# Kernel optimization log

Hardware: AMD Instinct MI355X
Metric: run time of the kernel (lower is better)

The kernel has to match this reference:

```python
import jax, jax.numpy as jnp
import numpy as np

B, N, DIM = 4, 4096, 1024
HEADS, DIM_HEAD = 16, 64
DIM_INNER = HEADS * DIM_HEAD
ATTN_SCALE = 8.0
EPS = 1e-12  # F.normalize default eps


def setup_inputs() -> dict:
    key = jax.random.key(0)
    k1, k2, k3, k4, k5 = jax.random.split(key, 5)
    x = jax.random.normal(k1, (B, N, DIM), dtype=jnp.float32)
    gamma = jnp.ones((DIM,), dtype=jnp.float32)
    # stored as (in, out) so forward is x @ w
    w_qkv = jax.random.normal(k2, (DIM, 3 * DIM_INNER), dtype=jnp.float32) * (DIM ** -0.5)
    temperature = jnp.ones((HEADS, 1, 1), dtype=jnp.float32)
    w_out = jax.random.normal(k3, (DIM_INNER, DIM), dtype=jnp.float32) * (DIM_INNER ** -0.5)
    return {"x": x, "gamma": gamma, "w_qkv": w_qkv, "temperature": temperature, "w_out": w_out}


def _l2norm(t):
    # F.normalize(t, dim=-1): t / max(||t||_2, eps)
    n = jnp.linalg.norm(t, axis=-1, keepdims=True)
    return t / jnp.maximum(n, EPS)


def reference(x, gamma, w_qkv, temperature, w_out):
    b, n, dim = x.shape
    # RMSNorm: F.normalize(x, dim=-1) * sqrt(dim) * gamma
    xn = _l2norm(x) * (dim ** 0.5) * gamma
    # QKV projection -> qkv b h d n
    qkv = (xn @ w_qkv).reshape(b, n, 3, HEADS, DIM_HEAD)
    qkv = qkv.transpose(2, 0, 3, 4, 1)  # (3, b, h, d, n)
    q, k, v = qkv[0], qkv[1], qkv[2]
    # l2-normalize q, k over the sequence (last) axis; temperature-scale q
    q = _l2norm(q) * jnp.exp(temperature)  # temperature: (h,1,1) broadcast
    k = _l2norm(k)
    # cross-covariance attention over the small channel dim d
    sim = jnp.einsum('bhdn,bhen->bhde', q, k) * ATTN_SCALE
    attn = jax.nn.softmax(sim, axis=-1)
    out = jnp.einsum('bhde,bhen->bhdn', attn, v)
    # b h d n -> b n (h d), then out projection
    out = out.transpose(0, 3, 1, 2).reshape(b, n, DIM_INNER)
    return out @ w_out
```

## Files before the change

kernel.cpp:

```cpp
#include <hip/hip_runtime.h>
#include <stdint.h>

typedef unsigned short u16;
typedef unsigned int u32;
typedef __attribute__((ext_vector_type(8))) __bf16 bf16x8;
typedef __attribute__((ext_vector_type(4))) float f32x4;

#define M_TOT 16384
#define DIMX  1024

__device__ __forceinline__ u16 f2b(float f) {
  u32 u = __builtin_bit_cast(u32, f);
  u32 r = (u + 0x7fffu + ((u >> 16) & 1u)) >> 16;
  return (u16)r;
}

__device__ __forceinline__ void gl2lds16(const void* g, void* l) {
  __builtin_amdgcn_global_load_lds((const __attribute__((address_space(1))) void*)g,
                                   (__attribute__((address_space(3))) void*)l,
                                   16, 0, 0);
}

__global__ __launch_bounds__(256) void k_rms(const float* __restrict__ x,
                                             const float* __restrict__ gamma,
                                             u16* __restrict__ xn) {
  int row = blockIdx.x;
  int t = threadIdx.x;
  const float4* xr = (const float4*)(x + (size_t)row * DIMX);
  float4 v = xr[t];
  float ss = v.x * v.x + v.y * v.y + v.z * v.z + v.w * v.w;
#pragma unroll
  for (int o = 32; o > 0; o >>= 1) ss += __shfl_xor(ss, o, 64);
  __shared__ float wss[4];
  int w = t >> 6;
  if ((t & 63) == 0) wss[w] = ss;
  __syncthreads();
  float tot = wss[0] + wss[1] + wss[2] + wss[3];
  float scale = 32.0f / fmaxf(sqrtf(tot), 1e-12f);
  float4 g = ((const float4*)gamma)[t];
  ushort4 o4;
  o4.x = f2b(v.x * scale * g.x);
  o4.y = f2b(v.y * scale * g.y);
  o4.z = f2b(v.z * scale * g.z);
  o4.w = f2b(v.w * scale * g.w);
  ((ushort4*)xn)[(size_t)row * 256 + t] = o4;
}

__global__ __launch_bounds__(256) void k_castT(const float* __restrict__ in,
                                               u16* __restrict__ out, int Rr, int Cc) {
  __shared__ float tile[32][33];
  int c0 = blockIdx.x * 32, r0 = blockIdx.y * 32;
  int tx = threadIdx.x, ty = threadIdx.y;
#pragma unroll
  for (int i = 0; i < 4; i++)
    tile[ty + i * 8][tx] = in[(size_t)(r0 + ty + i * 8) * Cc + c0 + tx];
  __syncthreads();
#pragma unroll
  for (int i = 0; i < 4; i++)
    out[(size_t)(c0 + ty + i * 8) * Rr + r0 + tx] = f2b(tile[tx][ty + i * 8]);
}


template<bool SWAP>
__device__ __forceinline__ f32x4 mf(bf16x8 a, bf16x8 b, f32x4 c) {
  return SWAP ? __builtin_amdgcn_mfma_f32_16x16x32_bf16(b, a, c, 0, 0, 0)
              : __builtin_amdgcn_mfma_f32_16x16x32_bf16(a, b, c, 0, 0, 0);
}

__device__ __forceinline__ void stage_half(const u16* __restrict__ g,
                                           u16* dst, int t, int k0) {
#pragma unroll
  for (int r = 0; r < 2; r++) {
    int chunk = r * 512 + t;
    int row = chunk >> 3;
    int cc = (chunk & 7) ^ (row & 7);
    gl2lds16(g + (size_t)row * 1024 + (k0 + cc * 8),
             dst + (r * 512 + (t >> 6) * 64) * 8);
  }
}

template<bool SWAP>
__device__ __forceinline__ void gemm_core256(const u16* __restrict__ Ag,
                                             const u16* __restrict__ Bg,
                                             u16* lds, int t, f32x4 (&acc)[8][4]) {
  const int lane = t & 63;
  const int r16 = lane & 15, q = lane >> 4;
  const int s0 = (q ^ (r16 & 7)) * 8;
  const int wr = (t >> 6) >> 2, wc = (t >> 6) & 3;
  const int arow = wr * 16 + r16;
  const int brow = wc * 16 + r16;

  stage_half(Ag,              lds + 0,     t, 0);
  stage_half(Bg,              lds + 16384, t, 0);
  stage_half(Bg + 128 * 1024, lds + 24576, t, 0);
  stage_half(Ag + 128 * 1024, lds + 8192,  t, 0);
  asm volatile("s_waitcnt vmcnt(4)" ::: "memory");
  __builtin_amdgcn_s_barrier();

  bf16x8 af[4][2], bl[2][2], bh[2][2];
#pragma unroll 1
  for (int tt = 0; tt < 16; tt++) {
    const int bo = (tt & 1) << 15;
    const int nb = bo ^ 32768;
    const int k1 = ((tt + 1) & 15) << 6;
    const u16* A0 = lds + bo;
    const u16* A1 = lds + bo + 8192;
    const u16* B0 = lds + bo + 16384;
    const u16* B1 = lds + bo + 24576;

#pragma unroll
    for (int i = 0; i < 4; i++) {
      af[i][0] = *(const bf16x8*)(A0 + (i * 32 + arow) * 64 + s0);
      af[i][1] = *(const bf16x8*)(A0 + (i * 32 + arow) * 64 + (s0 ^ 32));
    }
#pragma unroll
    for (int j = 0; j < 2; j++) {
      bl[j][0] = *(const bf16x8*)(B0 + (j * 64 + brow) * 64 + s0);
      bl[j][1] = *(const bf16x8*)(B0 + (j * 64 + brow) * 64 + (s0 ^ 32));
    }
    stage_half(Ag, lds + nb, t, k1);
    __builtin_amdgcn_s_setprio(1);
#pragma unroll
    for (int kq = 0; kq < 2; kq++)
#pragma unroll
      for (int i = 0; i < 4; i++)
#pragma unroll
        for (int j = 0; j < 2; j++)
          acc[i][j] = mf<SWAP>(af[i][kq], bl[j][kq], acc[i][j]);
    __builtin_amdgcn_s_setprio(0);
    asm volatile("s_waitcnt vmcnt(4)" ::: "memory");
    __builtin_amdgcn_s_barrier();

#pragma unroll
    for (int j = 0; j < 2; j++) {
      bh[j][0] = *(const bf16x8*)(B1 + (j * 64 + brow) * 64 + s0);
      bh[j][1] = *(const bf16x8*)(B1 + (j * 64 + brow) * 64 + (s0 ^ 32));
    }
    stage_half(Bg, lds + nb + 16384, t, k1);
    __builtin_amdgcn_s_setprio(1);
#pragma unroll
    for (int kq = 0; kq < 2; kq++)
#pragma unroll
      for (int i = 0; i < 4; i++)
#pragma unroll
        for (int j = 0; j < 2; j++)
          acc[i][2 + j] = mf<SWAP>(af[i][kq], bh[j][kq], acc[i][2 + j]);
    __builtin_amdgcn_s_setprio(0);
    asm volatile("s_waitcnt vmcnt(4)" ::: "memory");
    __builtin_amdgcn_s_barrier();

#pragma unroll
    for (int i = 0; i < 4; i++) {
      af[i][0] = *(const bf16x8*)(A1 + (i * 32 + arow) * 64 + s0);
      af[i][1] = *(const bf16x8*)(A1 + (i * 32 + arow) * 64 + (s0 ^ 32));
    }
    stage_half(Bg + 128 * 1024, lds + nb + 24576, t, k1);
    __builtin_amdgcn_s_setprio(1);
#pragma unroll
    for (int kq = 0; kq < 2; kq++)
#pragma unroll
      for (int i = 0; i < 4; i++)
#pragma unroll
        for (int j = 0; j < 2; j++)
          acc[4 + i][j] = mf<SWAP>(af[i][kq], bl[j][kq], acc[4 + i][j]);
    __builtin_amdgcn_s_setprio(0);
    __builtin_amdgcn_s_barrier();

    stage_half(Ag + 128 * 1024, lds + nb + 8192, t, k1);
    __builtin_amdgcn_s_setprio(1);
#pragma unroll
    for (int kq = 0; kq < 2; kq++)
#pragma unroll
      for (int i = 0; i < 4; i++)
#pragma unroll
        for (int j = 0; j < 2; j++)
          acc[4 + i][2 + j] = mf<SWAP>(af[i][kq], bh[j][kq], acc[4 + i][2 + j]);
    __builtin_amdgcn_s_setprio(0);
    asm volatile("s_waitcnt vmcnt(4)" ::: "memory");
    __builtin_amdgcn_s_barrier();
  }
}

__global__ __launch_bounds__(512, 2) void k_gemm1(const u16* __restrict__ A,
                                                  const u16* __restrict__ Bt,
                                                  u16* __restrict__ qkT,
                                                  u16* __restrict__ vmat,
                                                  float* __restrict__ sumsq) {
  __shared__ u16 lds[8 * 8192];
  int l = blockIdx.x;
  int xcd = l & 7, c = l >> 3;
  int mt = xcd * 8 + (c & 7);
  int nt = c >> 3;
  int m0 = mt * 256, n0 = nt * 256;
  int t = threadIdx.x, lane = t & 63;
  int r16 = lane & 15, q = lane >> 4;
  int wr = (t >> 6) >> 2, wc = (t >> 6) & 3;
  f32x4 acc[8][4] = {};
  if (n0 < 2048) {
    gemm_core256<false>(A + (size_t)m0 * 1024, Bt + (size_t)n0 * 1024, lds, t, acc);
    int b = m0 >> 12;
#pragma unroll
    for (int j = 0; j < 4; j++) {
      int cc = n0 + j * 64 + wc * 16 + r16;
      float colss = 0.f;
#pragma unroll
      for (int i = 0; i < 8; i++) {
        f32x4 a = acc[i][j];
        colss += a.x * a.x + a.y * a.y + a.z * a.z + a.w * a.w;
        int m = m0 + i * 32 + wr * 16 + q * 4;
        ushort4 o4;
        o4.x = f2b(a.x); o4.y = f2b(a.y); o4.z = f2b(a.z); o4.w = f2b(a.w);
        *(ushort4*)(qkT + (size_t)cc * M_TOT + m) = o4;
      }
      colss += __shfl_xor(colss, 16, 64);
      colss += __shfl_xor(colss, 32, 64);
      if (lane < 16) atomicAdd(&sumsq[b * 2048 + cc], colss);
    }
  } else {
    gemm_core256<true>(A + (size_t)m0 * 1024, Bt + (size_t)n0 * 1024, lds, t, acc);
    int vc0 = n0 - 2048;
#pragma unroll
    for (int i = 0; i < 8; i++) {
      int m = m0 + i * 32 + wr * 16 + r16;
#pragma unroll
      for (int j = 0; j < 4; j++) {
        int cc = vc0 + j * 64 + wc * 16 + q * 4;
        f32x4 a = acc[i][j];
        ushort4 o4;
        o4.x = f2b(a.x); o4.y = f2b(a.y); o4.z = f2b(a.z); o4.w = f2b(a.w);
        *(ushort4*)(vmat + (size_t)m * 1024 + cc) = o4;
      }
    }
  }
}

__global__ __launch_bounds__(256) void k_attn_s(const u16* __restrict__ qkT,
                                                float* __restrict__ Spart) {
  __shared__ u16 Ql[64 * 256];
  __shared__ u16 Kl[64 * 256];
  int bh = blockIdx.x, split = blockIdx.y;
  int b = bh >> 4, h = bh & 15;
  int t = threadIdx.x, lane = t & 63, w = t >> 6;
  int r16 = lane & 15, q = lane >> 4;
  const u16* qbase = qkT + (size_t)(h * 64) * M_TOT + b * 4096 + split * 1024;
  const u16* kbase = qkT + (size_t)(1024 + h * 64) * M_TOT + b * 4096 + split * 1024;
  int drow = w * 16 + r16;
  f32x4 acc[4] = {};
#pragma unroll 1
  for (int it = 0; it < 4; it++) {
    int ncol = it * 256;
#pragma unroll
    for (int r = 0; r < 8; r++) {
      int ch = r * 256 + t;
      int row = ch >> 5;
      int sl = (ch & 31) ^ (row & 31);
      gl2lds16(qbase + (size_t)row * M_TOT + ncol + sl * 8,
               Ql + (r * 256 + w * 64) * 8);
      gl2lds16(kbase + (size_t)row * M_TOT + ncol + sl * 8,
               Kl + (r * 256 + w * 64) * 8);
    }
    asm volatile("s_waitcnt vmcnt(0)" ::: "memory");
    __syncthreads();
#pragma unroll
    for (int it2 = 0; it2 < 8; it2++) {
      bf16x8 aq = *(const bf16x8*)(Ql + drow * 256 + (((it2 * 4 + q) ^ (drow & 31)) * 8));
#pragma unroll
      for (int j = 0; j < 4; j++) {
        int erow = j * 16 + r16;
        bf16x8 bk = *(const bf16x8*)(Kl + erow * 256 + (((it2 * 4 + q) ^ (erow & 31)) * 8));
        acc[j] = __builtin_amdgcn_mfma_f32_16x16x32_bf16(bk, aq, acc[j], 0, 0, 0);
      }
    }
    __syncthreads();
  }
  float* Sp = Spart + ((size_t)split * 64 + bh) * 4096;
#pragma unroll
  for (int j = 0; j < 4; j++)
    *(f32x4*)(Sp + drow * 64 + j * 16 + q * 4) = acc[j];
}

__global__ __launch_bounds__(256) void k_softmax(const float* __restrict__ Spart,
                                                 const float* __restrict__ sumsq,
                                                 const float* __restrict__ temp,
                                                 u16* __restrict__ PT) {
  int bh = blockIdx.x;
  int b = bh >> 4, h = bh & 15;
  int t = threadIdx.x;
  int d = t & 63, w = t >> 6;
  int e0 = w * 16;
  __shared__ float rnk[64];
  __shared__ float redm[4][64];
  __shared__ float reds[4][64];
  if (t < 64) rnk[t] = 1.0f / fmaxf(sqrtf(sumsq[b * 2048 + 1024 + h * 64 + t]), 1e-12f);
  __syncthreads();
  float nq = sqrtf(sumsq[b * 2048 + h * 64 + d]);
  float qs = 8.0f * __expf(temp[h]) / fmaxf(nq, 1e-12f);
  const float* Sp = Spart + (size_t)bh * 4096 + d * 64 + e0;
  float vals[16];
#pragma unroll
  for (int e = 0; e < 16; e += 4) {
    f32x4 v = {};
#pragma unroll
    for (int s = 0; s < 4; s++)
      v += *(const f32x4*)(Sp + (size_t)s * 64 * 4096 + e);
    vals[e + 0] = v.x; vals[e + 1] = v.y; vals[e + 2] = v.z; vals[e + 3] = v.w;
  }
  float mx = -3.0e38f;
#pragma unroll
  for (int e = 0; e < 16; e++) {
    float v = vals[e] * qs * rnk[e0 + e];
    vals[e] = v;
    mx = fmaxf(mx, v);
  }
  redm[w][d] = mx;
  __syncthreads();
  float M = fmaxf(fmaxf(redm[0][d], redm[1][d]), fmaxf(redm[2][d], redm[3][d]));
  float s = 0.f;
#pragma unroll
  for (int e = 0; e < 16; e++) {
    float v = __expf(vals[e] - M);
    vals[e] = v;
    s += v;
  }
  reds[w][d] = s;
  __syncthreads();
  float inv = 1.0f / (reds[0][d] + reds[1][d] + reds[2][d] + reds[3][d]);
#pragma unroll
  for (int e = 0; e < 16; e++)
    PT[((size_t)bh * 64 + e0 + e) * 64 + d] = f2b(vals[e] * inv);
}

__global__ __launch_bounds__(256) void k_m(const u16* __restrict__ woT,
                                           const u16* __restrict__ PT,
                                           u16* __restrict__ MT) {
  int bh = blockIdx.x;
  int b = bh >> 4, h = bh & 15;
  int o0 = blockIdx.y * 128;
  int t = threadIdx.x, lane = t & 63, w = t >> 6;
  int r16 = lane & 15, q = lane >> 4;
  const u16* pbase = PT + (size_t)bh * 4096;
  f32x4 acc[2][4] = {};
#pragma unroll
  for (int ks = 0; ks < 2; ks++) {
    int kk = ks * 32 + q * 8;
    bf16x8 af[2], bfr[4];
#pragma unroll
    for (int i = 0; i < 2; i++)
      af[i] = *(const bf16x8*)(woT + (size_t)(o0 + w * 32 + i * 16 + r16) * 1024 + h * 64 + kk);
#pragma unroll
    for (int j = 0; j < 4; j++)
      bfr[j] = *(const bf16x8*)(pbase + (size_t)(j * 16 + r16) * 64 + kk);
#pragma unroll
    for (int i = 0; i < 2; i++)
#pragma unroll
      for (int j = 0; j < 4; j++)
        acc[i][j] = __builtin_amdgcn_mfma_f32_16x16x32_bf16(af[i], bfr[j], acc[i][j], 0, 0, 0);
  }
  u16* dst = MT + (size_t)b * 1024 * 1024;
#pragma unroll
  for (int i = 0; i < 2; i++) {
    int o = o0 + w * 32 + i * 16 + q * 4;
#pragma unroll
    for (int j = 0; j < 4; j++) {
      int e = h * 64 + j * 16 + r16;
      f32x4 a = acc[i][j];
      dst[(size_t)(o + 0) * 1024 + e] = f2b(a.x);
      dst[(size_t)(o + 1) * 1024 + e] = f2b(a.y);
      dst[(size_t)(o + 2) * 1024 + e] = f2b(a.z);
      dst[(size_t)(o + 3) * 1024 + e] = f2b(a.w);
    }
  }
}

__global__ __launch_bounds__(512, 2) void k_gemm2(const u16* __restrict__ A,
                                                  const u16* __restrict__ Bt,
                                                  float* __restrict__ C) {
  __shared__ u16 lds[8 * 8192];
  int l = blockIdx.x;
  int xcd = l & 7, c = l >> 3;
  int mt = xcd * 8 + (c & 7);
  int nt = c >> 3;
  int m0 = mt * 256, n0 = nt * 256;
  int b = m0 >> 12;
  const u16* Bb = Bt + (size_t)b * 1024 * 1024;
  int t = threadIdx.x, lane = t & 63;
  int r16 = lane & 15, q = lane >> 4;
  int wr = (t >> 6) >> 2, wc = (t >> 6) & 3;
  f32x4 acc[8][4] = {};
  gemm_core256<true>(A + (size_t)m0 * 1024, Bb + (size_t)n0 * 1024, lds, t, acc);
#pragma unroll
  for (int i = 0; i < 8; i++) {
    int m = m0 + i * 32 + wr * 16 + r16;
#pragma unroll
    for (int j = 0; j < 4; j++) {
      int cc = n0 + j * 64 + wc * 16 + q * 4;
      *(f32x4*)(C + (size_t)m * 1024 + cc) = acc[i][j];
    }
  }
}

extern "C" void kernel_launch(void* const* d_in, const int* in_sizes, int n_in,
                              void* d_out, int out_size, void* d_ws, size_t ws_size,
                              hipStream_t stream) {
  const float* x     = (const float*)d_in[0];
  const float* gamma = (const float*)d_in[1];
  const float* wqkv  = (const float*)d_in[2];
  const float* temp  = (const float*)d_in[3];
  const float* wout  = (const float*)d_in[4];
  float* out = (float*)d_out;

  char* ws = (char*)d_ws;
  size_t off = 0;
  u16* xn = (u16*)(ws + off);    off += (size_t)M_TOT * 1024 * 2;
  u16* wqT = (u16*)(ws + off);   off += (size_t)3072 * 1024 * 2;
  u16* woT = (u16*)(ws + off);   off += (size_t)1024 * 1024 * 2;
  u16* qkT = (u16*)(ws + off);   off += (size_t)2048 * M_TOT * 2;
  u16* vmat = (u16*)(ws + off);  off += (size_t)M_TOT * 1024 * 2;
  float* sumsq = (float*)(ws + off); off += (size_t)4 * 2048 * 4;
  u16* PT = (u16*)(ws + off);    off += (size_t)64 * 64 * 64 * 2;
  u16* MT = (u16*)(ws + off);    off += (size_t)4 * 1024 * 1024 * 2;

  float* Spart = (float*)xn;

  hipMemsetAsync((void*)sumsq, 0, (size_t)4 * 2048 * 4, stream);

  k_rms<<<16384, 256, 0, stream>>>(x, gamma, xn);
  dim3 cb(32, 8);
  k_castT<<<dim3(3072 / 32, 1024 / 32), cb, 0, stream>>>(wqkv, wqT, 1024, 3072);
  k_castT<<<dim3(1024 / 32, 1024 / 32), cb, 0, stream>>>(wout, woT, 1024, 1024);
  k_gemm1<<<768, 512, 0, stream>>>(xn, wqT, qkT, vmat, sumsq);
  k_attn_s<<<dim3(64, 4), 256, 0, stream>>>(qkT, Spart);
  k_softmax<<<64, 256, 0, stream>>>(Spart, sumsq, temp, PT);
  k_m<<<dim3(64, 8), 256, 0, stream>>>(woT, PT, MT);
  k_gemm2<<<1024 / 4, 512, 0, stream>>>(vmat, MT, out);
}
```

Measured before the change: 309.2 us.

## Replace 256x256 GEMM tiles with simpler 128x128 double-buffered tiles

Both projection GEMMs move from a 256x256 block tile with 8 waves and a four-phase interleaved pipeline to a 128x128 tile with 4 waves and a plain double-buffered loop that waits for all loads each k-step. The grids grow fourfold to 3072 and 1024 blocks, giving more blocks per CU and better load balance, and each block uses half the LDS. In exchange, every operand is re-read from global/L2 twice as often, and the full vmcnt(0) wait reduces overlap between loads and MFMA work.

```diff
diff --git a/kernel.cpp b/kernel.cpp
--- a/kernel.cpp
+++ b/kernel.cpp
@@ -67,147 +67,92 @@
               : __builtin_amdgcn_mfma_f32_16x16x32_bf16(a, b, c, 0, 0, 0);
 }
 
-__device__ __forceinline__ void stage_half(const u16* __restrict__ g,
-                                           u16* dst, int t, int k0) {
-#pragma unroll
-  for (int r = 0; r < 2; r++) {
-    int chunk = r * 512 + t;
-    int row = chunk >> 3;
-    int cc = (chunk & 7) ^ (row & 7);
-    gl2lds16(g + (size_t)row * 1024 + (k0 + cc * 8),
-             dst + (r * 512 + (t >> 6) * 64) * 8);
+__device__ __forceinline__ void stage128(const u16* __restrict__ g,
+                                         u16* dst, int t, int k0) {
+#pragma unroll
+  for (int r = 0; r < 4; r++) {
+    int c = r * 256 + t;
+    int row = c >> 3;
+    int sl = (c & 7) ^ (row & 7);
+    gl2lds16(g + (size_t)row * 1024 + k0 + sl * 8,
+             dst + (r * 256 + (t >> 6) * 64) * 8);
   }
 }
 
 template<bool SWAP>
-__device__ __forceinline__ void gemm_core256(const u16* __restrict__ Ag,
+__device__ __forceinline__ void gemm_core128(const u16* __restrict__ Ag,
                                              const u16* __restrict__ Bg,
-                                             u16* lds, int t, f32x4 (&acc)[8][4]) {
+                                             u16* lds, int t, f32x4 (&acc)[4][4]) {
   const int lane = t & 63;
   const int r16 = lane & 15, q = lane >> 4;
   const int s0 = (q ^ (r16 & 7)) * 8;
-  const int wr = (t >> 6) >> 2, wc = (t >> 6) & 3;
-  const int arow = wr * 16 + r16;
-  const int brow = wc * 16 + r16;
-
-  stage_half(Ag,              lds + 0,     t, 0);
-  stage_half(Bg,              lds + 16384, t, 0);
-  stage_half(Bg + 128 * 1024, lds + 24576, t, 0);
-  stage_half(Ag + 128 * 1024, lds + 8192,  t, 0);
-  asm volatile("s_waitcnt vmcnt(4)" ::: "memory");
+  const int wr = (t >> 6) >> 1, wc = (t >> 6) & 1;
+  const int arow = wr * 64 + r16;
+  const int brow = wc * 64 + r16;
+
+  stage128(Ag, lds + 0,    t, 0);
+  stage128(Bg, lds + 8192, t, 0);
+  asm volatile("s_waitcnt vmcnt(0)" ::: "memory");
   __builtin_amdgcn_s_barrier();
 
-  bf16x8 af[4][2], bl[2][2], bh[2][2];
+  bf16x8 af[4][2], bf[4][2];
 #pragma unroll 1
   for (int tt = 0; tt < 16; tt++) {
-    const int bo = (tt & 1) << 15;
-    const int nb = bo ^ 32768;
+    const int bo = (tt & 1) << 14;
+    const int nb = bo ^ 16384;
     const int k1 = ((tt + 1) & 15) << 6;
-    const u16* A0 = lds + bo;
-    const u16* A1 = lds + bo + 8192;
-    const u16* B0 = lds + bo + 16384;
-    const u16* B1 = lds + bo + 24576;
-
+    stage128(Ag, lds + nb,        t, k1);
+    stage128(Bg, lds + nb + 8192, t, k1);
+    const u16* A = lds + bo;
+    const u16* B = lds + bo + 8192;
 #pragma unroll
     for (int i = 0; i < 4; i++) {
-      af[i][0] = *(const bf16x8*)(A0 + (i * 32 + arow) * 64 + s0);
-      af[i][1] = *(const bf16x8*)(A0 + (i * 32 + arow) * 64 + (s0 ^ 32));
-    }
-#pragma unroll
-    for (int j = 0; j < 2; j++) {
-      bl[j][0] = *(const bf16x8*)(B0 + (j * 64 + brow) * 64 + s0);
-      bl[j][1] = *(const bf16x8*)(B0 + (j * 64 + brow) * 64 + (s0 ^ 32));
-    }
-    stage_half(Ag, lds + nb, t, k1);
+      af[i][0] = *(const bf16x8*)(A + (i * 16 + arow) * 64 + s0);
+      af[i][1] = *(const bf16x8*)(A + (i * 16 + arow) * 64 + (s0 ^ 32));
+      bf[i][0] = *(const bf16x8*)(B + (i * 16 + brow) * 64 + s0);
+      bf[i][1] = *(const bf16x8*)(B + (i * 16 + brow) * 64 + (s0 ^ 32));
+    }
     __builtin_amdgcn_s_setprio(1);
 #pragma unroll
     for (int kq = 0; kq < 2; kq++)
 #pragma unroll
       for (int i = 0; i < 4; i++)
 #pragma unroll
-        for (int j = 0; j < 2; j++)
-          acc[i][j] = mf<SWAP>(af[i][kq], bl[j][kq], acc[i][j]);
+        for (int j = 0; j < 4; j++)
+          acc[i][j] = mf<SWAP>(af[i][kq], bf[j][kq], acc[i][j]);
     __builtin_amdgcn_s_setprio(0);
-    asm volatile("s_waitcnt vmcnt(4)" ::: "memory");
+    asm volatile("s_waitcnt vmcnt(0)" ::: "memory");
     __builtin_amdgcn_s_barrier();
-
-#pragma unroll
-    for (int j = 0; j < 2; j++) {
-      bh[j][0] = *(const bf16x8*)(B1 + (j * 64 + brow) * 64 + s0);
-      bh[j][1] = *(const bf16x8*)(B1 + (j * 64 + brow) * 64 + (s0 ^ 32));
-    }
-    stage_half(Bg, lds + nb + 16384, t, k1);
-    __builtin_amdgcn_s_setprio(1);
-#pragma unroll
-    for (int kq = 0; kq < 2; kq++)
-#pragma unroll
-      for (int i = 0; i < 4; i++)
-#pragma unroll
-        for (int j = 0; j < 2; j++)
-          acc[i][2 + j] = mf<SWAP>(af[i][kq], bh[j][kq], acc[i][2 + j]);
-    __builtin_amdgcn_s_setprio(0);
-    asm volatile("s_waitcnt vmcnt(4)" ::: "memory");
-    __builtin_amdgcn_s_barrier();
-
-#pragma unroll
-    for (int i = 0; i < 4; i++) {
-      af[i][0] = *(const bf16x8*)(A1 + (i * 32 + arow) * 64 + s0);
-      af[i][1] = *(const bf16x8*)(A1 + (i * 32 + arow) * 64 + (s0 ^ 32));
-    }
-    stage_half(Bg + 128 * 1024, lds + nb + 24576, t, k1);
-    __builtin_amdgcn_s_setprio(1);
-#pragma unroll
-    for (int kq = 0; kq < 2; kq++)
-#pragma unroll
-      for (int i = 0; i < 4; i++)
-#pragma unroll
-        for (int j = 0; j < 2; j++)
-          acc[4 + i][j] = mf<SWAP>(af[i][kq], bl[j][kq], acc[4 + i][j]);
-    __builtin_amdgcn_s_setprio(0);
-    __builtin_amdgcn_s_barrier();
-
-    stage_half(Ag + 128 * 1024, lds + nb + 8192, t, k1);
-    __builtin_amdgcn_s_setprio(1);
-#pragma unroll
-    for (int kq = 0; kq < 2; kq++)
-#pragma unroll
-      for (int i = 0; i < 4; i++)
-#pragma unroll
-        for (int j = 0; j < 2; j++)
-          acc[4 + i][2 + j] = mf<SWAP>(af[i][kq], bh[j][kq], acc[4 + i][2 + j]);
-    __builtin_amdgcn_s_setprio(0);
-    asm volatile("s_waitcnt vmcnt(4)" ::: "memory");
-    __builtin_amdgcn_s_barrier();
-  }
-}
-
-__global__ __launch_bounds__(512, 2) void k_gemm1(const u16* __restrict__ A,
+  }
+}
+
+__global__ __launch_bounds__(256, 2) void k_gemm1(const u16* __restrict__ A,
                                                   const u16* __restrict__ Bt,
                                                   u16* __restrict__ qkT,
                                                   u16* __restrict__ vmat,
                                                   float* __restrict__ sumsq) {
-  __shared__ u16 lds[8 * 8192];
+  __shared__ u16 lds[2 * 16384];
   int l = blockIdx.x;
   int xcd = l & 7, c = l >> 3;
-  int mt = xcd * 8 + (c & 7);
-  int nt = c >> 3;
-  int m0 = mt * 256, n0 = nt * 256;
+  int mt = xcd * 16 + (c & 15);
+  int nt = c >> 4;
+  int m0 = mt * 128, n0 = nt * 128;
   int t = threadIdx.x, lane = t & 63;
   int r16 = lane & 15, q = lane >> 4;
-  int wr = (t >> 6) >> 2, wc = (t >> 6) & 3;
-  f32x4 acc[8][4] = {};
+  int wr = (t >> 6) >> 1, wc = (t >> 6) & 1;
+  f32x4 acc[4][4] = {};
   if (n0 < 2048) {
-    gemm_core256<false>(A + (size_t)m0 * 1024, Bt + (size_t)n0 * 1024, lds, t, acc);
+    gemm_core128<false>(A + (size_t)m0 * 1024, Bt + (size_t)n0 * 1024, lds, t, acc);
     int b = m0 >> 12;
 #pragma unroll
     for (int j = 0; j < 4; j++) {
-      int cc = n0 + j * 64 + wc * 16 + r16;
+      int cc = n0 + wc * 64 + j * 16 + r16;
       float colss = 0.f;
 #pragma unroll
-      for (int i = 0; i < 8; i++) {
+      for (int i = 0; i < 4; i++) {
         f32x4 a = acc[i][j];
         colss += a.x * a.x + a.y * a.y + a.z * a.z + a.w * a.w;
-        int m = m0 + i * 32 + wr * 16 + q * 4;
+        int m = m0 + wr * 64 + i * 16 + q * 4;
         ushort4 o4;
         o4.x = f2b(a.x); o4.y = f2b(a.y); o4.z = f2b(a.z); o4.w = f2b(a.w);
         *(ushort4*)(qkT + (size_t)cc * M_TOT + m) = o4;
@@ -217,14 +162,14 @@
       if (lane < 16) atomicAdd(&sumsq[b * 2048 + cc], colss);
     }
   } else {
-    gemm_core256<true>(A + (size_t)m0 * 1024, Bt + (size_t)n0 * 1024, lds, t, acc);
+    gemm_core128<true>(A + (size_t)m0 * 1024, Bt + (size_t)n0 * 1024, lds, t, acc);
     int vc0 = n0 - 2048;
 #pragma unroll
-    for (int i = 0; i < 8; i++) {
-      int m = m0 + i * 32 + wr * 16 + r16;
+    for (int i = 0; i < 4; i++) {
+      int m = m0 + wr * 64 + i * 16 + r16;
 #pragma unroll
       for (int j = 0; j < 4; j++) {
-        int cc = vc0 + j * 64 + wc * 16 + q * 4;
+        int cc = vc0 + wc * 64 + j * 16 + q * 4;
         f32x4 a = acc[i][j];
         ushort4 o4;
         o4.x = f2b(a.x); o4.y = f2b(a.y); o4.z = f2b(a.z); o4.w = f2b(a.w);
@@ -372,28 +317,28 @@
   }
 }
 
-__global__ __launch_bounds__(512, 2) void k_gemm2(const u16* __restrict__ A,
+__global__ __launch_bounds__(256, 2) void k_gemm2(const u16* __restrict__ A,
                                                   const u16* __restrict__ Bt,
                                                   float* __restrict__ C) {
-  __shared__ u16 lds[8 * 8192];
+  __shared__ u16 lds[2 * 16384];
   int l = blockIdx.x;
   int xcd = l & 7, c = l >> 3;
-  int mt = xcd * 8 + (c & 7);
-  int nt = c >> 3;
-  int m0 = mt * 256, n0 = nt * 256;
+  int mt = xcd * 16 + (c & 15);
+  int nt = c >> 4;
+  int m0 = mt * 128, n0 = nt * 128;
   int b = m0 >> 12;
   const u16* Bb = Bt + (size_t)b * 1024 * 1024;
   int t = threadIdx.x, lane = t & 63;
   int r16 = lane & 15, q = lane >> 4;
-  int wr = (t >> 6) >> 2, wc = (t >> 6) & 3;
-  f32x4 acc[8][4] = {};
-  gemm_core256<true>(A + (size_t)m0 * 1024, Bb + (size_t)n0 * 1024, lds, t, acc);
-#pragma unroll
-  for (int i = 0; i < 8; i++) {
-    int m = m0 + i * 32 + wr * 16 + r16;
+  int wr = (t >> 6) >> 1, wc = (t >> 6) & 1;
+  f32x4 acc[4][4] = {};
+  gemm_core128<true>(A + (size_t)m0 * 1024, Bb + (size_t)n0 * 1024, lds, t, acc);
+#pragma unroll
+  for (int i = 0; i < 4; i++) {
+    int m = m0 + wr * 64 + i * 16 + r16;
 #pragma unroll
     for (int j = 0; j < 4; j++) {
-      int cc = n0 + j * 64 + wc * 16 + q * 4;
+      int cc = n0 + wc * 64 + j * 16 + q * 4;
       *(f32x4*)(C + (size_t)m * 1024 + cc) = acc[i][j];
     }
   }
@@ -428,9 +373,9 @@
   dim3 cb(32, 8);
   k_castT<<<dim3(3072 / 32, 1024 / 32), cb, 0, stream>>>(wqkv, wqT, 1024, 3072);
   k_castT<<<dim3(1024 / 32, 1024 / 32), cb, 0, stream>>>(wout, woT, 1024, 1024);
-  k_gemm1<<<768, 512, 0, stream>>>(xn, wqT, qkT, vmat, sumsq);
+  k_gemm1<<<3072, 256, 0, stream>>>(xn, wqT, qkT, vmat, sumsq);
   k_attn_s<<<dim3(64, 4), 256, 0, stream>>>(qkT, Spart);
   k_softmax<<<64, 256, 0, stream>>>(Spart, sumsq, temp, PT);
   k_m<<<dim3(64, 8), 256, 0, stream>>>(woT, PT, MT);
-  k_gemm2<<<1024 / 4, 512, 0, stream>>>(vmat, MT, out);
-}
+  k_gemm2<<<1024, 256, 0, stream>>>(vmat, MT, out);
+}
```

New measurement: 311.1 us. No clear change (+0.6%).
